# Optimization experiments

Measured on AMD Instinct MI355X. Metric: run time of the kernel, lower is better.

## Reference

```python
import jax, jax.numpy as jnp
import numpy as np

B, S = 256, 512
NQ = 1000           # n_skills
MEM, DK, DV, FC = 20, 50, 200, 50  # memory_size, key dim, value dim, final fc dim


def _kaiming(key, shape, fan_in):
    return jax.random.normal(key, shape) * np.float32(np.sqrt(2.0 / fan_in))


def setup_inputs() -> dict:
    key = jax.random.key(0)
    ks = jax.random.split(key, 12)
    q_data = jax.random.randint(ks[0], (B, S), 0, NQ + 1)
    qa_data = jax.random.randint(ks[1], (B, S), 0, 2 * NQ + 1)
    u = jax.random.uniform(ks[2], (B * S,))
    # target: -1 = masked/padding, else binary label (matches target.ge(0) masking)
    target = jnp.where(u < 0.1, -1.0, (u > 0.55).astype(jnp.float32))
    q_embed_w = _kaiming(ks[3], (NQ + 1, DK), DK)
    qa_embed_w = _kaiming(ks[4], (2 * NQ + 1, DV), DV)
    memory_key = _kaiming(ks[5], (MEM, DK), DK)
    init_memory_value = _kaiming(ks[6], (MEM, DV), DV)
    erase_w = _kaiming(ks[7], (DV, DV), DV)
    erase_b = jnp.zeros((DV,), jnp.float32)
    add_w = _kaiming(ks[8], (DV, DV), DV)
    add_b = jnp.zeros((DV,), jnp.float32)
    read_w = _kaiming(ks[9], (DV + FC, FC), DV + FC)
    read_b = jnp.zeros((FC,), jnp.float32)
    pred_w = _kaiming(ks[10], (FC, 1), FC)
    pred_b = jnp.zeros((1,), jnp.float32)
    return dict(q_data=q_data, qa_data=qa_data, target=target,
                q_embed_w=q_embed_w, qa_embed_w=qa_embed_w,
                memory_key=memory_key, init_memory_value=init_memory_value,
                erase_w=erase_w, erase_b=erase_b, add_w=add_w, add_b=add_b,
                read_w=read_w, read_b=read_b, pred_w=pred_w, pred_b=pred_b)


def reference(q_data, qa_data, target, q_embed_w, qa_embed_w, memory_key,
              init_memory_value, erase_w, erase_b, add_w, add_b,
              read_w, read_b, pred_w, pred_b):
    b = q_data.shape[0]
    q_e = q_embed_w[q_data]     # [B,S,DK]
    qa_e = qa_embed_w[qa_data]  # [B,S,DV]
    Mv0 = jnp.broadcast_to(init_memory_value, (b, MEM, DV))

    def step(Mv, xs):
        q_t, qa_t = xs                                        # [B,DK], [B,DV]
        corr = jax.nn.softmax(q_t @ memory_key.T, axis=1)     # [B,MEM] addressing
        read = jnp.einsum('bm,bmd->bd', corr, Mv)             # weighted read
        erase = jax.nn.sigmoid(qa_t @ erase_w + erase_b)      # [B,DV]
        add = jnp.tanh(qa_t @ add_w + add_b)                  # [B,DV]
        w = corr[:, :, None]                                  # [B,MEM,1]
        Mv = Mv * (1.0 - w * erase[:, None, :]) + w * add[:, None, :]
        return Mv, read

    _, reads = jax.lax.scan(step, Mv0, (q_e.transpose(1, 0, 2), qa_e.transpose(1, 0, 2)))
    reads = reads.transpose(1, 0, 2)                          # [B,S,DV]
    x = jnp.concatenate([reads, q_e], axis=-1)                # [B,S,DV+FC]
    h = jnp.tanh(x @ read_w + read_b)                         # [B,S,FC]
    logits = (h @ pred_w + pred_b).reshape(-1)                # [B*S]
    mask = target >= 0.0
    t = jnp.where(mask, target, 0.0)
    # numerically-stable BCE-with-logits, masked mean
    bce = jnp.maximum(logits, 0.0) - logits * t + jnp.log1p(jnp.exp(-jnp.abs(logits)))
    loss = jnp.sum(jnp.where(mask, bce, 0.0)) / jnp.maximum(mask.sum(), 1)
    return loss, jax.nn.sigmoid(logits)
```

## Files before the change

### kernel.cpp

```cpp
#include <hip/hip_runtime.h>
#include <math.h>

#define B_   256
#define S_   512
#define NQ_  1000
#define MEM_ 20
#define DK_  50
#define DV_  200
#define FC_  50
#define RPB  2
#define CHK  16
#define CLEN (S_/CHK)
#define NKS  7
#define XS_STRIDE 232
#define NB_EA    1001
#define NB_CORR  4
#define NB_WPACK 7
#define NB_HQ    251
#define PREP_BLOCKS (NB_EA+NB_CORR+NB_WPACK+NB_HQ)
#define MM_BLOCKS (B_*CHK)

typedef __attribute__((ext_vector_type(8))) short bf16x8_t;
typedef __attribute__((ext_vector_type(4))) float f32x4_t;

static __device__ __forceinline__ unsigned short f2bf(float f){
  unsigned u = __float_as_uint(f);
  unsigned r = u + 0x7fffu + ((u >> 16) & 1u);
  return (unsigned short)(r >> 16);
}
static __device__ __forceinline__ float bf2f_lo(unsigned v){ return __uint_as_float(v << 16); }
static __device__ __forceinline__ float bf2f_hi(unsigned v){ return __uint_as_float(v & 0xffff0000u); }
static __device__ __forceinline__ float ftanh(float x){
  float e = __expf(2.f*x);
  return 1.f - 2.f*__builtin_amdgcn_rcpf(e+1.f);
}
static __device__ __forceinline__ float fsigm(float x){
  return __builtin_amdgcn_rcpf(1.f+__expf(-x));
}

__global__ __launch_bounds__(256) void k_prep(
    const float* __restrict__ qaw,
    const float* __restrict__ ew, const float* __restrict__ eb,
    const float* __restrict__ aw, const float* __restrict__ ab,
    float2* __restrict__ eaTab,
    const float* __restrict__ qw, const float* __restrict__ mk,
    float* __restrict__ corrTab,
    const float* __restrict__ rw, const float* __restrict__ rb,
    const float* __restrict__ pw,
    unsigned short* __restrict__ WpFrag, float* __restrict__ pwPad,
    float* __restrict__ hq){
  __shared__ float qa[RPB*DV_];
  int blk = blockIdx.x;
  if(blk < NB_EA){
    int row0 = blk*RPB;
    for(int i=threadIdx.x; i<RPB*DV_; i+=256){
      int r = i/DV_, cc = i - r*DV_;
      int row = row0 + r;
      qa[i] = (row <= 2*NQ_) ? qaw[row*DV_+cc] : 0.f;
    }
    __syncthreads();
    int d = threadIdx.x;
    if(d >= DV_) return;
    float accE[RPB], accA[RPB];
    #pragma unroll
    for(int r=0;r<RPB;++r){ accE[r] = eb[d]; accA[r] = ab[d]; }
    for(int j=0;j<DV_;++j){
      float we = ew[j*DV_+d], wa = aw[j*DV_+d];
      #pragma unroll
      for(int r=0;r<RPB;++r){
        float x = qa[r*DV_+j];
        accE[r] = fmaf(x, we, accE[r]);
        accA[r] = fmaf(x, wa, accA[r]);
      }
    }
    #pragma unroll
    for(int r=0;r<RPB;++r){
      int row = row0 + r;
      if(row <= 2*NQ_)
        eaTab[(size_t)row*DV_+d] = make_float2(fsigm(accE[r]), ftanh(accA[r]));
    }
  } else if(blk < NB_EA+NB_CORR){
    int q = (blk-NB_EA)*256 + threadIdx.x;
    if(q > NQ_) return;
    float qv[DK_];
    #pragma unroll
    for(int j=0;j<DK_;++j) qv[j] = qw[q*DK_+j];
    float s[MEM_]; float mx = -1e30f;
    #pragma unroll
    for(int m=0;m<MEM_;++m){
      float acc = 0.f;
      #pragma unroll
      for(int j=0;j<DK_;++j) acc = fmaf(qv[j], mk[m*DK_+j], acc);
      s[m] = acc; mx = fmaxf(mx, acc);
    }
    float sum = 0.f;
    #pragma unroll
    for(int m=0;m<MEM_;++m){ s[m] = __expf(s[m]-mx); sum += s[m]; }
    float inv = __builtin_amdgcn_rcpf(sum);
    #pragma unroll
    for(int m=0;m<MEM_;++m) corrTab[q*MEM_+m] = s[m]*inv;
  } else if(blk < NB_EA+NB_CORR+NB_WPACK){
    int ks = blk - (NB_EA+NB_CORR);
    int nt = threadIdx.x >> 6;
    int lane = threadIdx.x & 63;
    int quad = lane >> 4, col = lane & 15;
    int n = nt*16 + col;
    unsigned short tmp[8];
    #pragma unroll
    for(int j=0;j<8;++j){
      int k = ks*32 + quad*8 + j;
      tmp[j] = (k < DV_ && n < FC_) ? f2bf(rw[k*FC_+n]) : (unsigned short)0;
    }
    uint4* dst = reinterpret_cast<uint4*>(WpFrag + ((size_t)(ks*4+nt)*64 + lane)*8);
    *dst = *reinterpret_cast<const uint4*>(tmp);
    if(ks == 0 && threadIdx.x < 64)
      pwPad[threadIdx.x] = (threadIdx.x < FC_) ? pw[threadIdx.x] : 0.f;
  } else {
    int idx = (blk-(NB_EA+NB_CORR+NB_WPACK))*256 + threadIdx.x;
    int q = idx >> 6, n = idx & 63;
    if(q > NQ_) return;
    float v = 0.f;
    if(n < FC_){
      float acc = rb[n];
      #pragma unroll
      for(int j=0;j<DK_;++j)
        acc = fmaf(qw[q*DK_+j], rw[(DV_+j)*FC_+n], acc);
      v = acc;
    }
    hq[q*64+n] = v;
  }
}

__global__ __launch_bounds__(256) void k_scanA(const int* __restrict__ qd,
    const int* __restrict__ qad,
    const float4* __restrict__ corr4,
    const float2* __restrict__ eaTab,
    unsigned* __restrict__ ABu){
  const int blk = blockIdx.x;
  const int b = blk / (CHK-1), c = blk % (CHK-1);
  const int d = threadIdx.x;
  const int dc = (d < DV_) ? d : DV_-1;
  const bool act = (d < DV_);
  const int* __restrict__ qp  = qd  + b*S_ + c*CLEN;
  const int* __restrict__ qap = qad + b*S_ + c*CLEN;

  float A[MEM_], Bv[MEM_];
  #pragma unroll
  for(int m=0;m<MEM_;++m){ A[m] = 1.f; Bv[m] = 0.f; }

  int q2  = qp[1];
  int qa2 = qap[1];
  int q1  = qp[0];
  int qa1 = qap[0];
  float4 c0 = corr4[q1*5+0], c1 = corr4[q1*5+1], c2 = corr4[q1*5+2],
         c3 = corr4[q1*5+3], c4 = corr4[q1*5+4];
  float2 ea = eaTab[(size_t)qa1*DV_ + dc];

  #pragma unroll 2
  for(int t=0;t<CLEN;++t){
    int t2 = (t+2 < CLEN) ? t+2 : CLEN-1;
    int q3 = qp[t2], qa3 = qap[t2];
    float4 n0 = corr4[q2*5+0], n1 = corr4[q2*5+1], n2 = corr4[q2*5+2],
           n3 = corr4[q2*5+3], n4 = corr4[q2*5+4];
    float2 ean = eaTab[(size_t)qa2*DV_ + dc];

    const float e = ea.x, a = ea.y;
    #define UPD(cv, mi) { \
      float al = fmaf(-(cv), e, 1.f); \
      float be = (cv)*a; \
      A[mi] *= al; \
      Bv[mi] = fmaf(al, Bv[mi], be); }
    UPD(c0.x, 0)  UPD(c0.y, 1)  UPD(c0.z, 2)  UPD(c0.w, 3)
    UPD(c1.x, 4)  UPD(c1.y, 5)  UPD(c1.z, 6)  UPD(c1.w, 7)
    UPD(c2.x, 8)  UPD(c2.y, 9)  UPD(c2.z,10)  UPD(c2.w,11)
    UPD(c3.x,12)  UPD(c3.y,13)  UPD(c3.z,14)  UPD(c3.w,15)
    UPD(c4.x,16)  UPD(c4.y,17)  UPD(c4.z,18)  UPD(c4.w,19)
    #undef UPD

    c0=n0; c1=n1; c2=n2; c3=n3; c4=n4; ea=ean;
    q2=q3; qa2=qa3;
  }
  if(act){
    unsigned* base = ABu + ((size_t)(b*CHK + c)*MEM_)*DV_ + d;
    #pragma unroll
    for(int m=0;m<MEM_;++m)
      base[(size_t)m*DV_] = (unsigned)f2bf(A[m]) | ((unsigned)f2bf(Bv[m]) << 16);
  }
}

__global__ __launch_bounds__(256) void k_prefix(const float* __restrict__ mv0,
    unsigned* __restrict__ ABu){
  int i = blockIdx.x*256 + threadIdx.x;
  if(i >= B_*MEM_*DV_) return;
  int d = i % DV_;
  int m = (i / DV_) % MEM_;
  int b = i / (DV_*MEM_);
  unsigned abv[CHK-1];
  #pragma unroll
  for(int c=0;c<CHK-1;++c)
    abv[c] = ABu[((size_t)(b*CHK + c)*MEM_ + m)*DV_ + d];
  float Mv = mv0[m*DV_+d];
  #pragma unroll
  for(int c=0;c<CHK;++c){
    ABu[((size_t)(b*CHK + c)*MEM_ + m)*DV_ + d] = (unsigned)f2bf(Mv);
    if(c < CHK-1) Mv = fmaf(bf2f_lo(abv[c]), Mv, bf2f_hi(abv[c]));
  }
}

__global__ __launch_bounds__(256) void k_scan_mm(const int* __restrict__ qd,
    const int* __restrict__ qad,
    const float4* __restrict__ corr4,
    const float2* __restrict__ eaTab,
    const unsigned* __restrict__ ABu,
    const unsigned short* __restrict__ WpFrag,
    const float* __restrict__ hq,
    const float* __restrict__ pwPad, const float* __restrict__ pb,
    const float* __restrict__ target,
    float* __restrict__ out, float2* __restrict__ partials){
  __shared__ unsigned short Xs[CLEN*XS_STRIDE];
  __shared__ float sred[2][2][16];
  __shared__ float sbce[4];

  const int blk = blockIdx.x;
  const int b = blk >> 4, c = blk & (CHK-1);
  const int d = threadIdx.x;
  const int dc = (d < DV_) ? d : DV_-1;
  const bool act = (d < DV_);
  const bool pad = (d < 224);
  const int* __restrict__ qp  = qd  + b*S_ + c*CLEN;
  const int* __restrict__ qap = qad + b*S_ + c*CLEN;

  float Mv[MEM_];
  {
    const unsigned* base = ABu + ((size_t)(b*CHK + c)*MEM_)*DV_ + dc;
    #pragma unroll
    for(int m=0;m<MEM_;++m) Mv[m] = bf2f_lo(base[(size_t)m*DV_]);
  }

  int q2  = qp[1];
  int qa2 = qap[1];
  int q1  = qp[0];
  int qa1 = qap[0];
  float4 c0 = corr4[q1*5+0], c1 = corr4[q1*5+1], c2 = corr4[q1*5+2],
         c3 = corr4[q1*5+3], c4 = corr4[q1*5+4];
  float2 ea = eaTab[(size_t)qa1*DV_ + dc];

  #pragma unroll 2
  for(int t=0;t<CLEN;++t){
    int t2 = (t+2 < CLEN) ? t+2 : CLEN-1;
    int q3 = qp[t2], qa3 = qap[t2];
    float4 n0 = corr4[q2*5+0], n1 = corr4[q2*5+1], n2 = corr4[q2*5+2],
           n3 = corr4[q2*5+3], n4 = corr4[q2*5+4];
    float2 ean = eaTab[(size_t)qa2*DV_ + dc];

    const float e = ea.x, a = ea.y;
    float rd = 0.f;
    #define UPD(cv, mi) \
      rd = fmaf(cv, Mv[mi], rd); \
      Mv[mi] = fmaf(cv, fmaf(-Mv[mi], e, a), Mv[mi]);
    UPD(c0.x, 0)  UPD(c0.y, 1)  UPD(c0.z, 2)  UPD(c0.w, 3)
    UPD(c1.x, 4)  UPD(c1.y, 5)  UPD(c1.z, 6)  UPD(c1.w, 7)
    UPD(c2.x, 8)  UPD(c2.y, 9)  UPD(c2.z,10)  UPD(c2.w,11)
    UPD(c3.x,12)  UPD(c3.y,13)  UPD(c3.z,14)  UPD(c3.w,15)
    UPD(c4.x,16)  UPD(c4.y,17)  UPD(c4.z,18)  UPD(c4.w,19)
    #undef UPD

    if(pad) Xs[t*XS_STRIDE + d] = act ? f2bf(rd) : (unsigned short)0;

    c0=n0; c1=n1; c2=n2; c3=n3; c4=n4; ea=ean;
    q2=q3; qa2=qa3;
  }
  __syncthreads();

  const int wave = threadIdx.x >> 6;
  const int lane = threadIdx.x & 63;
  const int col  = lane & 15, quad = lane >> 4;
  const int rt   = wave & 1;
  const int nh   = wave >> 1;
  const int mbase = rt*16;

  f32x4_t acc[2];
  acc[0] = (f32x4_t){0.f,0.f,0.f,0.f};
  acc[1] = (f32x4_t){0.f,0.f,0.f,0.f};

  #pragma unroll
  for(int ks=0;ks<NKS;++ks){
    bf16x8_t a = *reinterpret_cast<const bf16x8_t*>(Xs + (mbase+col)*XS_STRIDE + quad*8 + ks*32);
    #pragma unroll
    for(int j=0;j<2;++j){
      int nt = nh*2 + j;
      bf16x8_t bfr = *reinterpret_cast<const bf16x8_t*>(WpFrag + ((size_t)(ks*4+nt)*64 + lane)*8);
      acc[j] = __builtin_amdgcn_mfma_f32_16x16x32_bf16(a, bfr, acc[j], 0, 0, 0);
    }
  }

  float part[4];
  #pragma unroll
  for(int reg=0;reg<4;++reg){
    int mloc = mbase + quad*4 + reg;
    int q = qp[mloc];
    float s = 0.f;
    #pragma unroll
    for(int j=0;j<2;++j){
      int n = (nh*2+j)*16 + col;
      float h = acc[j][reg] + hq[q*64 + n];
      s = fmaf(pwPad[n], ftanh(h), s);
    }
    part[reg] = s;
  }
  #pragma unroll
  for(int off=1; off<16; off<<=1){
    #pragma unroll
    for(int reg=0;reg<4;++reg) part[reg] += __shfl_xor(part[reg], off, 64);
  }
  if(col == 0){
    #pragma unroll
    for(int reg=0;reg<4;++reg) sred[rt][nh][quad*4+reg] = part[reg];
  }
  __syncthreads();

  float bce = 0.f, cnt = 0.f;
  if(nh == 0 && col == 0){
    float pbv = pb[0];
    #pragma unroll
    for(int reg=0;reg<4;++reg){
      int idx = quad*4 + reg;
      int mloc = mbase + idx;
      int row = b*S_ + c*CLEN + mloc;
      float logit = sred[rt][0][idx] + sred[rt][1][idx] + pbv;
      out[1+row] = fsigm(logit);
      float t = target[row];
      if(t >= 0.f){
        cnt += 1.f;
        bce += fmaxf(logit,0.f) - logit*t + log1pf(__expf(-fabsf(logit)));
      }
    }
  }
  bce += __shfl_xor(bce, 16, 64); cnt += __shfl_xor(cnt, 16, 64);
  bce += __shfl_xor(bce, 32, 64); cnt += __shfl_xor(cnt, 32, 64);
  if(lane == 0 && nh == 0){ sbce[wave] = bce; sbce[2+wave] = cnt; }
  __syncthreads();
  if(threadIdx.x == 0)
    partials[blk] = make_float2(sbce[0]+sbce[1], sbce[2]+sbce[3]);
}

__global__ __launch_bounds__(256) void k_fin(const float2* __restrict__ partials,
                                             float* __restrict__ out){
  float bce = 0.f, cnt = 0.f;
  for(int i=threadIdx.x; i<MM_BLOCKS; i+=256){
    float2 p = partials[i];
    bce += p.x; cnt += p.y;
  }
  #pragma unroll
  for(int off=32; off>0; off>>=1){
    bce += __shfl_down(bce, off, 64);
    cnt += __shfl_down(cnt, off, 64);
  }
  __shared__ float sb[4], sc[4];
  int w = threadIdx.x >> 6;
  if((threadIdx.x & 63) == 0){ sb[w] = bce; sc[w] = cnt; }
  __syncthreads();
  if(threadIdx.x == 0){
    float Bt = sb[0]+sb[1]+sb[2]+sb[3];
    float Ct = sc[0]+sc[1]+sc[2]+sc[3];
    out[0] = Bt / fmaxf(Ct, 1.f);
  }
}

extern "C" void kernel_launch(void* const* d_in, const int* in_sizes, int n_in,
                              void* d_out, int out_size, void* d_ws, size_t ws_size,
                              hipStream_t stream){
  const int*   qd     = (const int*)d_in[0];
  const int*   qad    = (const int*)d_in[1];
  const float* target = (const float*)d_in[2];
  const float* qw     = (const float*)d_in[3];
  const float* qaw    = (const float*)d_in[4];
  const float* mk     = (const float*)d_in[5];
  const float* mv0    = (const float*)d_in[6];
  const float* ew     = (const float*)d_in[7];
  const float* eb     = (const float*)d_in[8];
  const float* aw     = (const float*)d_in[9];
  const float* ab     = (const float*)d_in[10];
  const float* rw     = (const float*)d_in[11];
  const float* rb     = (const float*)d_in[12];
  const float* pw     = (const float*)d_in[13];
  const float* pb     = (const float*)d_in[14];
  float* out = (float*)d_out;

  char* ws = (char*)d_ws;
  size_t off = 0;
  float2* partials = (float2*)(ws + off);            off += (size_t)MM_BLOCKS*8;
  float* corrTab  = (float*)(ws + off);              off += (((size_t)(NQ_+1)*MEM_*4 + 255)/256)*256;
  float2* eaTab   = (float2*)(ws + off);             off += (((size_t)(2*NQ_+1)*DV_*8 + 255)/256)*256;
  unsigned* ABu   = (unsigned*)(ws + off);           off += (size_t)B_*CHK*MEM_*DV_*4;
  unsigned short* WpFrag = (unsigned short*)(ws + off); off += ((size_t)NKS*4*64*8*2 + 255)/256*256;
  float* pwPad    = (float*)(ws + off);              off += 256;
  float* hq       = (float*)(ws + off);              off += (size_t)(NQ_+1)*64*4;

  k_prep<<<dim3(PREP_BLOCKS), dim3(256), 0, stream>>>(qaw, ew, eb, aw, ab, eaTab,
                                                      qw, mk, corrTab,
                                                      rw, rb, pw, WpFrag, pwPad, hq);
  k_scanA<<<dim3(B_*(CHK-1)), dim3(256), 0, stream>>>(qd, qad, (const float4*)corrTab, (const float2*)eaTab, ABu);
  k_prefix<<<dim3((B_*MEM_*DV_+255)/256), dim3(256), 0, stream>>>(mv0, ABu);
  k_scan_mm<<<dim3(MM_BLOCKS), dim3(256), 0, stream>>>(qd, qad, (const float4*)corrTab, (const float2*)eaTab,
                                                       ABu, WpFrag, hq, pwPad, pb, target, out, partials);
  k_fin<<<dim3(1), dim3(256), 0, stream>>>(partials, out);
}
```

Before: 247.4 us.

## Halve scan chunk count, widen MFMA tile per wave, fuse final loss reduction

Cuts the number of sequence chunks per batch row from 16 to 8, so each chunked-scan block handles 64 timesteps and the scanA/prefix stages carry fewer chunk transitions. Each wave now computes all four N-tiles of its own 16-row M tile, which removes the shared-memory cross-wave logit reduction and one barrier. Chunk start states go to a separate bf16 buffer instead of being written in place over ABu. The separate final-reduction kernel is replaced by a last-block-done atomic counter pattern, at the cost of a memset and fewer, longer-running blocks with less parallelism in the scan stage.

```diff
diff --git a/kernel.cpp b/kernel.cpp
--- a/kernel.cpp
+++ b/kernel.cpp
@@ -9,7 +9,7 @@
 #define DV_  200
 #define FC_  50
 #define RPB  2
-#define CHK  16
+#define CHK  8
 #define CLEN (S_/CHK)
 #define NKS  7
 #define XS_STRIDE 232
@@ -19,6 +19,7 @@
 #define NB_HQ    251
 #define PREP_BLOCKS (NB_EA+NB_CORR+NB_WPACK+NB_HQ)
 #define MM_BLOCKS (B_*CHK)
+#define SCANA_BLOCKS (B_*(CHK-1))
 
 typedef __attribute__((ext_vector_type(8))) short bf16x8_t;
 typedef __attribute__((ext_vector_type(4))) float f32x4_t;
@@ -181,7 +182,7 @@
     q2=q3; qa2=qa3;
   }
   if(act){
-    unsigned* base = ABu + ((size_t)(b*CHK + c)*MEM_)*DV_ + d;
+    unsigned* base = ABu + ((size_t)(b*(CHK-1) + c)*MEM_)*DV_ + d;
     #pragma unroll
     for(int m=0;m<MEM_;++m)
       base[(size_t)m*DV_] = (unsigned)f2bf(A[m]) | ((unsigned)f2bf(Bv[m]) << 16);
@@ -189,7 +190,7 @@
 }
 
 __global__ __launch_bounds__(256) void k_prefix(const float* __restrict__ mv0,
-    unsigned* __restrict__ ABu){
+    const unsigned* __restrict__ ABu, unsigned short* __restrict__ Mv0s){
   int i = blockIdx.x*256 + threadIdx.x;
   if(i >= B_*MEM_*DV_) return;
   int d = i % DV_;
@@ -198,11 +199,11 @@
   unsigned abv[CHK-1];
   #pragma unroll
   for(int c=0;c<CHK-1;++c)
-    abv[c] = ABu[((size_t)(b*CHK + c)*MEM_ + m)*DV_ + d];
+    abv[c] = ABu[((size_t)(b*(CHK-1) + c)*MEM_ + m)*DV_ + d];
   float Mv = mv0[m*DV_+d];
   #pragma unroll
   for(int c=0;c<CHK;++c){
-    ABu[((size_t)(b*CHK + c)*MEM_ + m)*DV_ + d] = (unsigned)f2bf(Mv);
+    Mv0s[((size_t)(b*CHK + c)*MEM_ + m)*DV_ + d] = f2bf(Mv);
     if(c < CHK-1) Mv = fmaf(bf2f_lo(abv[c]), Mv, bf2f_hi(abv[c]));
   }
 }
@@ -211,30 +212,32 @@
     const int* __restrict__ qad,
     const float4* __restrict__ corr4,
     const float2* __restrict__ eaTab,
-    const unsigned* __restrict__ ABu,
+    const unsigned short* __restrict__ Mv0s,
     const unsigned short* __restrict__ WpFrag,
     const float* __restrict__ hq,
     const float* __restrict__ pwPad, const float* __restrict__ pb,
     const float* __restrict__ target,
-    float* __restrict__ out, float2* __restrict__ partials){
+    float* __restrict__ out,
+    float* __restrict__ pbce, float* __restrict__ pcnt,
+    unsigned* __restrict__ counter){
   __shared__ unsigned short Xs[CLEN*XS_STRIDE];
-  __shared__ float sred[2][2][16];
-  __shared__ float sbce[4];
+  __shared__ float sbce[8];
+  __shared__ int lastBlk;
 
   const int blk = blockIdx.x;
-  const int b = blk >> 4, c = blk & (CHK-1);
+  const int b = blk >> 3, c = blk & (CHK-1);
   const int d = threadIdx.x;
   const int dc = (d < DV_) ? d : DV_-1;
   const bool act = (d < DV_);
-  const bool pad = (d < 224);
+  const bool padw = (d < 224);
   const int* __restrict__ qp  = qd  + b*S_ + c*CLEN;
   const int* __restrict__ qap = qad + b*S_ + c*CLEN;
 
   float Mv[MEM_];
   {
-    const unsigned* base = ABu + ((size_t)(b*CHK + c)*MEM_)*DV_ + dc;
-    #pragma unroll
-    for(int m=0;m<MEM_;++m) Mv[m] = bf2f_lo(base[(size_t)m*DV_]);
+    const unsigned short* base = Mv0s + ((size_t)(b*CHK + c)*MEM_)*DV_ + dc;
+    #pragma unroll
+    for(int m=0;m<MEM_;++m) Mv[m] = bf2f_lo((unsigned)base[(size_t)m*DV_]);
   }
 
   int q2  = qp[1];
@@ -265,7 +268,7 @@
     UPD(c4.x,16)  UPD(c4.y,17)  UPD(c4.z,18)  UPD(c4.w,19)
     #undef UPD
 
-    if(pad) Xs[t*XS_STRIDE + d] = act ? f2bf(rd) : (unsigned short)0;
+    if(padw) Xs[t*XS_STRIDE + d] = act ? f2bf(rd) : (unsigned short)0;
 
     c0=n0; c1=n1; c2=n2; c3=n3; c4=n4; ea=ean;
     q2=q3; qa2=qa3;
@@ -275,22 +278,19 @@
   const int wave = threadIdx.x >> 6;
   const int lane = threadIdx.x & 63;
   const int col  = lane & 15, quad = lane >> 4;
-  const int rt   = wave & 1;
-  const int nh   = wave >> 1;
-  const int mbase = rt*16;
-
-  f32x4_t acc[2];
-  acc[0] = (f32x4_t){0.f,0.f,0.f,0.f};
-  acc[1] = (f32x4_t){0.f,0.f,0.f,0.f};
+  const int mbase = wave*16;
+
+  f32x4_t acc[4];
+  #pragma unroll
+  for(int nt=0;nt<4;++nt) acc[nt] = (f32x4_t){0.f,0.f,0.f,0.f};
 
   #pragma unroll
   for(int ks=0;ks<NKS;++ks){
     bf16x8_t a = *reinterpret_cast<const bf16x8_t*>(Xs + (mbase+col)*XS_STRIDE + quad*8 + ks*32);
     #pragma unroll
-    for(int j=0;j<2;++j){
-      int nt = nh*2 + j;
+    for(int nt=0;nt<4;++nt){
       bf16x8_t bfr = *reinterpret_cast<const bf16x8_t*>(WpFrag + ((size_t)(ks*4+nt)*64 + lane)*8);
-      acc[j] = __builtin_amdgcn_mfma_f32_16x16x32_bf16(a, bfr, acc[j], 0, 0, 0);
+      acc[nt] = __builtin_amdgcn_mfma_f32_16x16x32_bf16(a, bfr, acc[nt], 0, 0, 0);
     }
   }
 
@@ -301,9 +301,9 @@
     int q = qp[mloc];
     float s = 0.f;
     #pragma unroll
-    for(int j=0;j<2;++j){
-      int n = (nh*2+j)*16 + col;
-      float h = acc[j][reg] + hq[q*64 + n];
+    for(int nt=0;nt<4;++nt){
+      int n = nt*16 + col;
+      float h = acc[nt][reg] + hq[q*64 + n];
       s = fmaf(pwPad[n], ftanh(h), s);
     }
     part[reg] = s;
@@ -313,21 +313,15 @@
     #pragma unroll
     for(int reg=0;reg<4;++reg) part[reg] += __shfl_xor(part[reg], off, 64);
   }
+
+  float bce = 0.f, cnt = 0.f;
   if(col == 0){
-    #pragma unroll
-    for(int reg=0;reg<4;++reg) sred[rt][nh][quad*4+reg] = part[reg];
-  }
-  __syncthreads();
-
-  float bce = 0.f, cnt = 0.f;
-  if(nh == 0 && col == 0){
     float pbv = pb[0];
     #pragma unroll
     for(int reg=0;reg<4;++reg){
-      int idx = quad*4 + reg;
-      int mloc = mbase + idx;
+      int mloc = mbase + quad*4 + reg;
       int row = b*S_ + c*CLEN + mloc;
-      float logit = sred[rt][0][idx] + sred[rt][1][idx] + pbv;
+      float logit = part[reg] + pbv;
       out[1+row] = fsigm(logit);
       float t = target[row];
       if(t >= 0.f){
@@ -338,32 +332,40 @@
   }
   bce += __shfl_xor(bce, 16, 64); cnt += __shfl_xor(cnt, 16, 64);
   bce += __shfl_xor(bce, 32, 64); cnt += __shfl_xor(cnt, 32, 64);
-  if(lane == 0 && nh == 0){ sbce[wave] = bce; sbce[2+wave] = cnt; }
+  if(lane == 0){ sbce[wave] = bce; sbce[4+wave] = cnt; }
   __syncthreads();
-  if(threadIdx.x == 0)
-    partials[blk] = make_float2(sbce[0]+sbce[1], sbce[2]+sbce[3]);
-}
-
-__global__ __launch_bounds__(256) void k_fin(const float2* __restrict__ partials,
-                                             float* __restrict__ out){
-  float bce = 0.f, cnt = 0.f;
-  for(int i=threadIdx.x; i<MM_BLOCKS; i+=256){
-    float2 p = partials[i];
-    bce += p.x; cnt += p.y;
-  }
-  #pragma unroll
-  for(int off=32; off>0; off>>=1){
-    bce += __shfl_down(bce, off, 64);
-    cnt += __shfl_down(cnt, off, 64);
-  }
-  __shared__ float sb[4], sc[4];
-  int w = threadIdx.x >> 6;
-  if((threadIdx.x & 63) == 0){ sb[w] = bce; sc[w] = cnt; }
+
+  if(threadIdx.x == 0){
+    float tb = sbce[0]+sbce[1]+sbce[2]+sbce[3];
+    float tc = sbce[4]+sbce[5]+sbce[6]+sbce[7];
+    __hip_atomic_store(&pbce[blk], tb, __ATOMIC_RELAXED, __HIP_MEMORY_SCOPE_AGENT);
+    __hip_atomic_store(&pcnt[blk], tc, __ATOMIC_RELAXED, __HIP_MEMORY_SCOPE_AGENT);
+    __threadfence();
+    unsigned old = __hip_atomic_fetch_add(counter, 1u, __ATOMIC_ACQ_REL, __HIP_MEMORY_SCOPE_AGENT);
+    lastBlk = (old == MM_BLOCKS-1);
+  }
   __syncthreads();
-  if(threadIdx.x == 0){
-    float Bt = sb[0]+sb[1]+sb[2]+sb[3];
-    float Ct = sc[0]+sc[1]+sc[2]+sc[3];
-    out[0] = Bt / fmaxf(Ct, 1.f);
+
+  if(lastBlk){
+    float rb_ = 0.f, rc_ = 0.f;
+    for(int i=threadIdx.x; i<MM_BLOCKS; i+=256){
+      rb_ += __hip_atomic_load(&pbce[i], __ATOMIC_RELAXED, __HIP_MEMORY_SCOPE_AGENT);
+      rc_ += __hip_atomic_load(&pcnt[i], __ATOMIC_RELAXED, __HIP_MEMORY_SCOPE_AGENT);
+    }
+    #pragma unroll
+    for(int off=32; off>0; off>>=1){
+      rb_ += __shfl_down(rb_, off, 64);
+      rc_ += __shfl_down(rc_, off, 64);
+    }
+    __shared__ float fb[4], fc[4];
+    int w = threadIdx.x >> 6;
+    if((threadIdx.x & 63) == 0){ fb[w] = rb_; fc[w] = rc_; }
+    __syncthreads();
+    if(threadIdx.x == 0){
+      float Bt = fb[0]+fb[1]+fb[2]+fb[3];
+      float Ct = fc[0]+fc[1]+fc[2]+fc[3];
+      out[0] = Bt / fmaxf(Ct, 1.f);
+    }
   }
 }
 
@@ -389,20 +391,24 @@
 
   char* ws = (char*)d_ws;
   size_t off = 0;
-  float2* partials = (float2*)(ws + off);            off += (size_t)MM_BLOCKS*8;
+  unsigned* counter = (unsigned*)(ws + off);         off += 256;
+  float* pbce     = (float*)(ws + off);              off += (size_t)MM_BLOCKS*4;
+  float* pcnt     = (float*)(ws + off);              off += (size_t)MM_BLOCKS*4;
   float* corrTab  = (float*)(ws + off);              off += (((size_t)(NQ_+1)*MEM_*4 + 255)/256)*256;
   float2* eaTab   = (float2*)(ws + off);             off += (((size_t)(2*NQ_+1)*DV_*8 + 255)/256)*256;
-  unsigned* ABu   = (unsigned*)(ws + off);           off += (size_t)B_*CHK*MEM_*DV_*4;
+  unsigned* ABu   = (unsigned*)(ws + off);           off += (size_t)SCANA_BLOCKS*MEM_*DV_*4;
+  unsigned short* Mv0s = (unsigned short*)(ws + off); off += (size_t)MM_BLOCKS*MEM_*DV_*2;
   unsigned short* WpFrag = (unsigned short*)(ws + off); off += ((size_t)NKS*4*64*8*2 + 255)/256*256;
   float* pwPad    = (float*)(ws + off);              off += 256;
   float* hq       = (float*)(ws + off);              off += (size_t)(NQ_+1)*64*4;
 
+  hipMemsetAsync(counter, 0, sizeof(unsigned), stream);
   k_prep<<<dim3(PREP_BLOCKS), dim3(256), 0, stream>>>(qaw, ew, eb, aw, ab, eaTab,
                                                       qw, mk, corrTab,
                                                       rw, rb, pw, WpFrag, pwPad, hq);
-  k_scanA<<<dim3(B_*(CHK-1)), dim3(256), 0, stream>>>(qd, qad, (const float4*)corrTab, (const float2*)eaTab, ABu);
-  k_prefix<<<dim3((B_*MEM_*DV_+255)/256), dim3(256), 0, stream>>>(mv0, ABu);
+  k_scanA<<<dim3(SCANA_BLOCKS), dim3(256), 0, stream>>>(qd, qad, (const float4*)corrTab, (const float2*)eaTab, ABu);
+  k_prefix<<<dim3((B_*MEM_*DV_+255)/256), dim3(256), 0, stream>>>(mv0, ABu, Mv0s);
   k_scan_mm<<<dim3(MM_BLOCKS), dim3(256), 0, stream>>>(qd, qad, (const float4*)corrTab, (const float2*)eaTab,
-                                                       ABu, WpFrag, hq, pwPad, pb, target, out, partials);
-  k_fin<<<dim3(1), dim3(256), 0, stream>>>(partials, out);
-}
+                                                       Mv0s, WpFrag, hq, pwPad, pb, target, out,
+                                                       pbce, pcnt, counter);
+}
```

After: 288.7 us. 16.7% more time.
